# Kernel tuning notes

Hardware: AMD Instinct MI355X
Metric: run time of the kernel (lower is better)

## Reference

```python
import jax, jax.numpy as jnp
import numpy as np

KH, KW = 5, 5  # hardcoded in the module's build()


def setup_inputs() -> dict:
    key = jax.random.key(0)
    k1, k2 = jax.random.split(key)
    # inputs are cast to int32 inside call(); use integer-valued floats so the
    # cast is meaningful (pixel-like values in [0, 256)).
    inputs = jax.random.randint(k1, (4, 224, 224, 16), 0, 256).astype(jnp.float32)
    # learned kernel, shape (5, 5, C_in, filters); small signed integer values
    kernel = jax.random.randint(k2, (5, 5, 16, 32), -8, 8).astype(jnp.float32)
    return {"inputs": inputs, "kernel": kernel}


def reference(inputs, kernel):
    # Faithful int32 math: cast inputs and kernel to int32 as in call().
    x = inputs.astype(jnp.int32)            # [B, H, W, C]
    k = kernel.astype(jnp.int32)            # [KH, KW, C, F]
    B, H, W, C = x.shape
    F = k.shape[-1]
    Ho, Wo = H - KH + 1, W - KW + 1         # VALID 2D cross-correlation
    # Per-(channel, filter) conv with NO reduction over channels: fuse the
    # C_in*F separate MyConv2D launches into one vectorized 25-tap accumulation.
    out = jnp.zeros((B, Ho, Wo, C, F), dtype=jnp.int32)
    for i in range(KH):
        for j in range(KW):
            out = out + x[:, i:i + Ho, j:j + Wo, :, None] * k[i, j, :, :]
    # tf.stack(filters, axis=2) then tf.stack(channels, axis=2) produces
    # output layout [B, Ho, C, F, Wo].
    out = jnp.transpose(out, (0, 1, 3, 4, 2))
    return out.astype(jnp.float32)
```

## Files before the change

### kernel.cpp

```cpp
#include <hip/hip_runtime.h>

#define KH 5
#define KW 5
#define CIN 16
#define NF 32
#define H 224
#define W 224
#define HO 220
#define WO 220
#define RPB 4
#define XROWS (RPB + KH - 1)
#define WPAD 32
#define NTILE (HO / RPB)
#define NBLK (CIN * NTILE * 4)
#define NXCD 8
#define CPX (NBLK / NXCD)

__global__ void transpose_weights(const float* __restrict__ Kw,
                                  float* __restrict__ Wt) {
    int idx = blockIdx.x * 256 + threadIdx.x;
    if (idx < KH * KW * CIN * NF) {
        const int tap = idx / (CIN * NF);
        const int rem = idx - tap * (CIN * NF);
        const int c   = rem >> 5;
        const int f   = rem & 31;
        Wt[((size_t)(c * NF) + f) * WPAD + tap] = Kw[idx];
    }
}

__device__ __forceinline__ void compute_store(
    const float (&xr)[XROWS][8], const float (&wk)[KH * KW],
    const uint32_t (&obase)[RPB], int f, float* __restrict__ O)
{
    float acc[RPB][4];
#pragma unroll
    for (int r = 0; r < RPB; ++r)
#pragma unroll
        for (int q = 0; q < 4; ++q) acc[r][q] = 0.0f;

#pragma unroll
    for (int i = 0; i < KH; ++i)
#pragma unroll
        for (int j = 0; j < KW; ++j) {
            const float w = wk[i * KW + j];
#pragma unroll
            for (int r = 0; r < RPB; ++r) {
                acc[r][0] += xr[r + i][j + 0] * w;
                acc[r][1] += xr[r + i][j + 1] * w;
                acc[r][2] += xr[r + i][j + 2] * w;
                acc[r][3] += xr[r + i][j + 3] * w;
            }
        }

#pragma unroll
    for (int r = 0; r < RPB; ++r)
        *(float4*)&O[obase[r] + (uint32_t)f * WO] =
            make_float4(acc[r][0], acc[r][1], acc[r][2], acc[r][3]);
}

__global__ __launch_bounds__(256) void conv2d_main(
    const float* __restrict__ X,
    const float* __restrict__ Wt,
    float* __restrict__ O)
{
    __shared__ float xs[XROWS * W];

    const int bid = blockIdx.x;
    const int l   = (bid & 7) * CPX + (bid >> 3);
    const int c   = l & 15;
    const int rest = l >> 4;
    const int hoT = rest % NTILE;
    const int b   = rest / NTILE;
    const int ho0 = hoT * RPB;
    const int t   = threadIdx.x;

    const uint32_t xoff = ((uint32_t)(b * H + ho0) * W) * CIN + c;
#pragma unroll
    for (int k = 0; k < XROWS * W / 256; ++k) {
        const int idx = t + k * 256;
        xs[idx] = X[xoff + (uint32_t)idx * CIN];
    }
    __syncthreads();

    const int wave = t >> 6;
    const int lane = t & 63;
    const int wo0  = lane * 4;
    if (lane >= 55) return;

    float xr[XROWS][8];
#pragma unroll
    for (int r = 0; r < XROWS; ++r) {
        const float4 xa = *(const float4*)&xs[r * W + wo0];
        const float4 xb = *(const float4*)&xs[r * W + wo0 + 4];
        xr[r][0] = xa.x; xr[r][1] = xa.y; xr[r][2] = xa.z; xr[r][3] = xa.w;
        xr[r][4] = xb.x; xr[r][5] = xb.y; xr[r][6] = xb.z; xr[r][7] = xb.w;
    }

    uint32_t obase[RPB];
#pragma unroll
    for (int r = 0; r < RPB; ++r)
        obase[r] = (((uint32_t)(b * HO + ho0 + r) * CIN + c) * NF) * WO + wo0;

    const float* wc = Wt + (size_t)(c * NF) * WPAD;
    const int f0 = __builtin_amdgcn_readfirstlane(wave * 8);

    float wkA[KH * KW], wkB[KH * KW];
    {
        const float* wp = wc + (size_t)f0 * WPAD;
#pragma unroll
        for (int tap = 0; tap < KH * KW; ++tap) wkA[tap] = wp[tap];
    }

#pragma unroll 1
    for (int fi = 0; fi < 8; fi += 2) {
        {
            const float* wp = wc + (size_t)(f0 + fi + 1) * WPAD;
#pragma unroll
            for (int tap = 0; tap < KH * KW; ++tap) wkB[tap] = wp[tap];
        }
        compute_store(xr, wkA, obase, f0 + fi, O);

        {
            const float* wp = wc + (size_t)(f0 + ((fi + 2) & 7)) * WPAD;
#pragma unroll
            for (int tap = 0; tap < KH * KW; ++tap) wkA[tap] = wp[tap];
        }
        compute_store(xr, wkB, obase, f0 + fi + 1, O);
    }
}

extern "C" void kernel_launch(void* const* d_in, const int* in_sizes, int n_in,
                              void* d_out, int out_size, void* d_ws, size_t ws_size,
                              hipStream_t stream) {
    const float* X  = (const float*)d_in[0];
    const float* Kw = (const float*)d_in[1];
    float* O        = (float*)d_out;
    float* Wt       = (float*)d_ws;

    transpose_weights<<<dim3(50), 256, 0, stream>>>(Kw, Wt);
    conv2d_main<<<dim3(NBLK), 256, 0, stream>>>(X, Wt, O);
}
```

Baseline: 408.1 us.

## Pre-transpose input to planar layout and run one-wave conv blocks

Adds a kernel that rearranges the NHWC input into a per-channel planar buffer in workspace. The main convolution then runs as 64-thread blocks, each handling one filter octet, and loads its input rows directly from global memory with float4 reads instead of strided gathers into shared memory. This removes the strided 16-float-stride loads and the block-level shared-memory stage, at the cost of an extra full-input transpose pass and four times as many blocks rereading overlapping rows. The old path is kept as a fallback when the workspace is too small.

```diff
diff --git a/kernel.cpp b/kernel.cpp
--- a/kernel.cpp
+++ b/kernel.cpp
@@ -4,6 +4,7 @@
 #define KW 5
 #define CIN 16
 #define NF 32
+#define BATCH 4
 #define H 224
 #define W 224
 #define HO 220
@@ -11,10 +12,16 @@
 #define RPB 4
 #define XROWS (RPB + KH - 1)
 #define WPAD 32
+
 #define NTILE (HO / RPB)
-#define NBLK (CIN * NTILE * 4)
-#define NXCD 8
-#define CPX (NBLK / NXCD)
+#define NBLKP (4 * CIN * NTILE * BATCH)
+#define CPXP (NBLKP / 8)
+
+#define NBLKL (CIN * NTILE * BATCH)
+#define CPXL (NBLKL / 8)
+
+#define XP_FLOATS ((size_t)CIN * BATCH * H * W)
+#define WS_NEEDED (65536 + XP_FLOATS * 4)
 
 __global__ void transpose_weights(const float* __restrict__ Kw,
                                   float* __restrict__ Wt) {
@@ -28,7 +35,30 @@
     }
 }
 
-__device__ __forceinline__ void compute_store(
+__global__ __launch_bounds__(256) void transpose_input(
+    const float* __restrict__ X, float* __restrict__ Xp)
+{
+    __shared__ float tile[W * 17];
+    const int h = blockIdx.x;
+    const int b = blockIdx.y;
+    const int t = threadIdx.x;
+    const float* in = X + ((size_t)(b * H + h) * W) * CIN;
+#pragma unroll
+    for (int k = 0; k < W * CIN / 256; ++k) {
+        const int idx = k * 256 + t;
+        tile[(idx >> 4) * 17 + (idx & 15)] = in[idx];
+    }
+    __syncthreads();
+#pragma unroll
+    for (int k = 0; k < W * CIN / 256; ++k) {
+        const int idx = k * 256 + t;
+        const int c = idx / W;
+        const int w = idx - c * W;
+        Xp[((uint32_t)(c * BATCH + b) * H + h) * W + w] = tile[w * 17 + c];
+    }
+}
+
+__device__ __forceinline__ void pcompute_store(
     const float (&xr)[XROWS][8], const float (&wk)[KH * KW],
     const uint32_t (&obase)[RPB], int f, float* __restrict__ O)
 {
@@ -58,7 +88,67 @@
             make_float4(acc[r][0], acc[r][1], acc[r][2], acc[r][3]);
 }
 
-__global__ __launch_bounds__(256) void conv2d_main(
+__global__ __launch_bounds__(64, 4) void conv2d_planar(
+    const float* __restrict__ Xp,
+    const float* __restrict__ Wt,
+    float* __restrict__ O)
+{
+    const int bid = blockIdx.x;
+    const int l   = (bid & 7) * CPXP + (bid >> 3);
+    const int oct = l & 3;
+    const int c   = (l >> 2) & 15;
+    const int rest = l >> 6;
+    const int hoT = rest % NTILE;
+    const int b   = rest / NTILE;
+    const int ho0 = hoT * RPB;
+
+    const int lane = threadIdx.x;
+    const int wo0  = lane * 4;
+    if (lane >= 55) return;
+
+    const uint32_t rbase = ((uint32_t)(c * BATCH + b) * H + ho0) * W + wo0;
+    float xr[XROWS][8];
+#pragma unroll
+    for (int r = 0; r < XROWS; ++r) {
+        const float4 xa = *(const float4*)&Xp[rbase + (uint32_t)r * W];
+        const float4 xb = *(const float4*)&Xp[rbase + (uint32_t)r * W + 4];
+        xr[r][0] = xa.x; xr[r][1] = xa.y; xr[r][2] = xa.z; xr[r][3] = xa.w;
+        xr[r][4] = xb.x; xr[r][5] = xb.y; xr[r][6] = xb.z; xr[r][7] = xb.w;
+    }
+
+    uint32_t obase[RPB];
+#pragma unroll
+    for (int r = 0; r < RPB; ++r)
+        obase[r] = (((uint32_t)(b * HO + ho0 + r) * CIN + c) * NF) * WO + wo0;
+
+    const float* wc = Wt + (size_t)(c * NF) * WPAD;
+    const int f0 = oct * 8;
+
+    float wkA[KH * KW], wkB[KH * KW];
+    {
+        const float* wp = wc + (size_t)f0 * WPAD;
+#pragma unroll
+        for (int tap = 0; tap < KH * KW; ++tap) wkA[tap] = wp[tap];
+    }
+
+#pragma unroll 1
+    for (int fi = 0; fi < 8; fi += 2) {
+        {
+            const float* wp = wc + (size_t)(f0 + fi + 1) * WPAD;
+#pragma unroll
+            for (int tap = 0; tap < KH * KW; ++tap) wkB[tap] = wp[tap];
+        }
+        pcompute_store(xr, wkA, obase, f0 + fi, O);
+        {
+            const float* wp = wc + (size_t)(f0 + ((fi + 2) & 7)) * WPAD;
+#pragma unroll
+            for (int tap = 0; tap < KH * KW; ++tap) wkA[tap] = wp[tap];
+        }
+        pcompute_store(xr, wkB, obase, f0 + fi + 1, O);
+    }
+}
+
+__global__ __launch_bounds__(256) void conv2d_legacy(
     const float* __restrict__ X,
     const float* __restrict__ Wt,
     float* __restrict__ O)
@@ -66,7 +156,7 @@
     __shared__ float xs[XROWS * W];
 
     const int bid = blockIdx.x;
-    const int l   = (bid & 7) * CPX + (bid >> 3);
+    const int l   = (bid & 7) * CPXL + (bid >> 3);
     const int c   = l & 15;
     const int rest = l >> 4;
     const int hoT = rest % NTILE;
@@ -118,14 +208,13 @@
 #pragma unroll
             for (int tap = 0; tap < KH * KW; ++tap) wkB[tap] = wp[tap];
         }
-        compute_store(xr, wkA, obase, f0 + fi, O);
-
+        pcompute_store(xr, wkA, obase, f0 + fi, O);
         {
             const float* wp = wc + (size_t)(f0 + ((fi + 2) & 7)) * WPAD;
 #pragma unroll
             for (int tap = 0; tap < KH * KW; ++tap) wkA[tap] = wp[tap];
         }
-        compute_store(xr, wkB, obase, f0 + fi + 1, O);
+        pcompute_store(xr, wkB, obase, f0 + fi + 1, O);
     }
 }
 
@@ -136,7 +225,13 @@
     const float* Kw = (const float*)d_in[1];
     float* O        = (float*)d_out;
     float* Wt       = (float*)d_ws;
+    float* Xp       = (float*)((char*)d_ws + 65536);
 
     transpose_weights<<<dim3(50), 256, 0, stream>>>(Kw, Wt);
-    conv2d_main<<<dim3(NBLK), 256, 0, stream>>>(X, Wt, O);
-}
+    if (ws_size >= WS_NEEDED) {
+        transpose_input<<<dim3(H, BATCH), 256, 0, stream>>>(X, Xp);
+        conv2d_planar<<<dim3(NBLKP), 64, 0, stream>>>(Xp, Wt, O);
+    } else {
+        conv2d_legacy<<<dim3(NBLKL), 256, 0, stream>>>(X, Wt, O);
+    }
+}
```

Result: slower. 475.0 us (+16.4%).
